# Kernel tuning notes

Hardware: AMD Instinct MI355X
Metric: run time of the kernel (lower is better)

Reference implementation:

```python
import jax, jax.numpy as jnp
import numpy as np

N = 100000   # n_nodes
E = 1000000  # n_edges
B = 2000     # batch of interactions
K = 20       # n_neighbors
D = 172      # memory/node/edge/embedding dim
T = 172      # time encoding dim
MSG = 2 * D + D + T  # 688, identity message function
HEADS = 2


def setup_inputs() -> dict:
    key = jax.random.key(0)
    ks = jax.random.split(key, 32)
    g = lambda i, shape, fan: jax.random.normal(ks[i], shape, jnp.float32) / np.float32(np.sqrt(fan))
    inp = {}
    inp['memory'] = jax.random.normal(ks[0], (N, D), jnp.float32)
    inp['messages'] = jax.random.normal(ks[1], (N, MSG), jnp.float32)
    inp['edge_features'] = jax.random.normal(ks[2], (E, D), jnp.float32)
    inp['edge_times'] = jax.random.uniform(ks[3], (B,), jnp.float32) * 10000.0
    inp['neighbor_times'] = jax.random.uniform(ks[4], (3 * B, K), jnp.float32) * 10000.0
    # TimeEncode init: w = 1 / 10^linspace(0, 9, T)
    inp['time_w'] = jnp.asarray(1.0 / 10.0 ** np.linspace(0, 9, T), jnp.float32)
    inp['time_b'] = jnp.zeros((T,), jnp.float32)
    # GRUCell params
    inp['gru_w_ih'] = g(5, (3 * D, MSG), MSG)
    inp['gru_w_hh'] = g(6, (3 * D, D), D)
    inp['gru_b_ih'] = jnp.zeros((3 * D,), jnp.float32)
    inp['gru_b_hh'] = jnp.zeros((3 * D,), jnp.float32)
    # temporal attention params: query = [feat||time], key = [feat||edge||time]
    inp['w_q'] = g(7, (D, D + T), D + T)
    inp['w_k'] = g(8, (D, D + D + T), D + D + T)
    inp['w_v'] = g(9, (D, D + D + T), D + D + T)
    inp['w_o'] = g(10, (D, D), D)
    # MergeLayer(attn_out, src_feat)
    inp['merge_w1'] = g(11, (D, 2 * D), 2 * D)
    inp['merge_b1'] = jnp.zeros((D,), jnp.float32)
    inp['merge_w2'] = g(12, (D, D), D)
    inp['merge_b2'] = jnp.zeros((D,), jnp.float32)
    # affinity MergeLayer -> scalar score
    inp['aff_w1'] = g(13, (D, 2 * D), 2 * D)
    inp['aff_b1'] = jnp.zeros((D,), jnp.float32)
    inp['aff_w2'] = g(14, (1, D), D)
    inp['aff_b2'] = jnp.zeros((1,), jnp.float32)
    inp['source_nodes'] = jax.random.randint(ks[15], (B,), 0, N, jnp.int32)
    inp['destination_nodes'] = jax.random.randint(ks[16], (B,), 0, N, jnp.int32)
    inp['negative_nodes'] = jax.random.randint(ks[17], (B,), 0, N, jnp.int32)
    inp['neighbors'] = jax.random.randint(ks[18], (3 * B, K), 0, N, jnp.int32)
    inp['neighbor_edge_idxs'] = jax.random.randint(ks[19], (3 * B, K), 0, E, jnp.int32)
    return inp


def reference(memory, messages, edge_features, edge_times, neighbor_times,
              time_w, time_b, gru_w_ih, gru_w_hh, gru_b_ih, gru_b_hh,
              w_q, w_k, w_v, w_o, merge_w1, merge_b1, merge_w2, merge_b2,
              aff_w1, aff_b1, aff_w2, aff_b2,
              source_nodes, destination_nodes, negative_nodes,
              neighbors, neighbor_edge_idxs):
    d = memory.shape[1]
    dh = d // HEADS
    k_nbr = neighbors.shape[1]

    def time_enc(t):  # TimeEncode: cos(t * w + b)
        return jnp.cos(t[..., None] * time_w + time_b)

    # --- GRU memory update from aggregated ('last') messages ---
    gi = messages @ gru_w_ih.T + gru_b_ih          # [N, 3D]
    gh = memory @ gru_w_hh.T + gru_b_hh            # [N, 3D]
    i_r, i_z, i_n = jnp.split(gi, 3, axis=-1)
    h_r, h_z, h_n = jnp.split(gh, 3, axis=-1)
    r = jax.nn.sigmoid(i_r + h_r)
    z = jax.nn.sigmoid(i_z + h_z)
    n = jnp.tanh(i_n + r * h_n)
    mem_upd = (1.0 - z) * n + z * memory           # [N, D]

    # --- temporal graph attention embedding (1 layer) ---
    nodes = jnp.concatenate([source_nodes, destination_nodes, negative_nodes])  # [3B]
    ts = jnp.concatenate([edge_times, edge_times, edge_times])                  # [3B]
    m = nodes.shape[0]
    src_feat = mem_upd[nodes]                                                   # [3B, D]
    q_in = jnp.concatenate([src_feat, time_enc(jnp.zeros_like(ts))], axis=-1)   # [3B, D+T]
    nbr_feat = mem_upd[neighbors]                                               # [3B, K, D]
    e_feat = edge_features[neighbor_edge_idxs]                                  # [3B, K, D]
    dt = ts[:, None] - neighbor_times                                           # [3B, K]
    k_in = jnp.concatenate([nbr_feat, e_feat, time_enc(dt)], axis=-1)           # [3B, K, 2D+T]

    q = (q_in @ w_q.T).reshape(m, HEADS, dh)
    kk = (k_in @ w_k.T).reshape(m, k_nbr, HEADS, dh)
    vv = (k_in @ w_v.T).reshape(m, k_nbr, HEADS, dh)
    scores = jnp.einsum('nhd,nkhd->nhk', q, kk) / np.float32(np.sqrt(dh))
    valid = (neighbors > 0)[:, None, :]            # node 0 is the pad node
    scores = jnp.where(valid, scores, jnp.float32(-1e9))
    attn = jax.nn.softmax(scores, axis=-1)
    ctx = jnp.einsum('nhk,nkhd->nhd', attn, vv).reshape(m, d) @ w_o.T
    h1 = jax.nn.relu(jnp.concatenate([ctx, src_feat], axis=-1) @ merge_w1.T + merge_b1)
    emb = h1 @ merge_w2.T + merge_b2               # [3B, D]

    # --- affinity score on (src,dst) and (src,neg) pairs ---
    b = source_nodes.shape[0]
    s_emb, d_emb, n_emb = emb[:b], emb[b:2 * b], emb[2 * b:]
    s_cat = jnp.concatenate([s_emb, s_emb], axis=0)
    d_cat = jnp.concatenate([d_emb, n_emb], axis=0)
    ah = jax.nn.relu(jnp.concatenate([s_cat, d_cat], axis=-1) @ aff_w1.T + aff_b1)
    prob = jax.nn.sigmoid((ah @ aff_w2.T + aff_b2).squeeze(-1))  # [2B]
    return prob[:b], prob[b:]
```

## Files before the change

### kernel.cpp

```cpp
#include <hip/hip_runtime.h>
#include <math.h>

#define N_NODES 100000
#define BATCH   2000
#define KNBR    20
#define DF      172
#define MSGD    688
#define M3      6000
#define DH      86
#define KIN_D   516

#define KA      864
#define JP      768
#define KREAL   860
#define KSTEPS  (KA / 32)
#define NTILES_N ((N_NODES + 127) / 128)
#define NWG_GRU (NTILES_N * 6)

#define NKV     120000
#define KP_KV   544
#define JKV     384
#define KVS     352
#define NKV_TILES ((NKV + 127) / 128)
#define NKV_ROWS (NKV_TILES * 128)
#define NWG_KV  (NKV_TILES * 3)
#define KSTEPS_KV (KP_KV / 32)

typedef __bf16 bf16x8 __attribute__((ext_vector_type(8)));
typedef __bf16 bf16x4 __attribute__((ext_vector_type(4)));
typedef float  f32x4  __attribute__((ext_vector_type(4)));

#define WPB_OFF   0
#define BP4_OFF   331776
#define WKV_OFF   332544
#define MU_OFF    436992
#define UNI_OFF   17636992
#define KV_OFF    UNI_OFF
#define QB_OFF    38756992
#define CAT_OFF   39286400
#define EMBB_OFF  40922752
#define MW1O_OFF  41812608
#define WQB_OFF   41842192
#define WM1B_OFF  41875984
#define WM2B_OFF  41909776
#define WAFFB_OFF 41928208
#define BM1P_OFF  41962000
#define BM2P_OFF  41962192
#define BAFFP_OFF 41962384
#define NODES_OFF 41962768
#define KIN_OFF   42000000

__device__ __forceinline__ float sigmoidf_(float x) { return 1.0f / (1.0f + expf(-x)); }

typedef __attribute__((address_space(1))) const void gvoid;
typedef __attribute__((address_space(3))) void svoid;
__device__ __forceinline__ void gl16(const void* g, void* l) {
    __builtin_amdgcn_global_load_lds((gvoid*)g, (svoid*)l, 16, 0, 0);
}

__global__ __launch_bounds__(256) void prep_kernel(
    const float* __restrict__ w_ih, const float* __restrict__ w_hh,
    const float* __restrict__ b_ih, const float* __restrict__ b_hh,
    __bf16* __restrict__ wpb, float* __restrict__ bp4)
{
    int idx = blockIdx.x * 256 + threadIdx.x;
    if (idx < JP * KA) {
        int j = idx / KA, k = idx - j * KA;
        int d = j >> 2, g = j & 3;
        float v = 0.f;
        if (d < DF) {
            if (g == 0) {
                if (k < MSGD) v = w_ih[d * MSGD + k];
                else if (k < KREAL) v = w_hh[d * DF + (k - MSGD)];
            } else if (g == 1) {
                if (k < MSGD) v = w_ih[(d + DF) * MSGD + k];
                else if (k < KREAL) v = w_hh[(d + DF) * DF + (k - MSGD)];
            } else if (g == 2) {
                if (k < MSGD) v = w_ih[(d + 2 * DF) * MSGD + k];
            } else {
                if (k >= MSGD && k < KREAL) v = w_hh[(d + 2 * DF) * DF + (k - MSGD)];
            }
        }
        wpb[idx] = (__bf16)v;
    }
    if (idx < JP) {
        int d = idx >> 2, g = idx & 3;
        float b = 0.f;
        if (d < DF) {
            if (g == 0) b = b_ih[d] + b_hh[d];
            else if (g == 1) b = b_ih[d + DF] + b_hh[d + DF];
            else if (g == 2) b = b_ih[d + 2 * DF];
            else            b = b_hh[d + 2 * DF];
        }
        bp4[idx] = b;
    }
}

__global__ __launch_bounds__(256) void prep_kv_kernel(
    const float* __restrict__ w_k, const float* __restrict__ w_v,
    __bf16* __restrict__ wkvb)
{
    int idx = blockIdx.x * 256 + threadIdx.x;
    if (idx < JKV * KP_KV) {
        int j = idx / KP_KV, k = idx - j * KP_KV;
        float v = 0.f;
        if (k < KIN_D) {
            if (j < DF) v = w_k[j * KIN_D + k];
            else if (j >= 192 && j < 192 + DF) v = w_v[(j - 192) * KIN_D + k];
        }
        wkvb[idx] = (__bf16)v;
    }
}

__global__ __launch_bounds__(256) void conv_kernel(
    const float* __restrict__ messages, const float* __restrict__ memory,
    __bf16* __restrict__ xb)
{
    const long total = (long)N_NODES * (KA / 8);
    for (long idx = (long)blockIdx.x * 256 + threadIdx.x; idx < total;
         idx += (long)gridDim.x * 256) {
        const int r  = (int)(idx / (KA / 8));
        const int k  = (int)(idx - (long)r * (KA / 8)) * 8;
        float f[8];
        if (k < MSGD) {
            const float4 a = *(const float4*)(messages + (size_t)r * MSGD + k);
            const float4 b = *(const float4*)(messages + (size_t)r * MSGD + k + 4);
            f[0]=a.x; f[1]=a.y; f[2]=a.z; f[3]=a.w;
            f[4]=b.x; f[5]=b.y; f[6]=b.z; f[7]=b.w;
        } else {
            const int o = k - MSGD;
            const float4 a = *(const float4*)(memory + (size_t)r * DF + o);
            float4 b = make_float4(0.f, 0.f, 0.f, 0.f);
            if (o <= 164) b = *(const float4*)(memory + (size_t)r * DF + o + 4);
            f[0]=a.x; f[1]=a.y; f[2]=a.z; f[3]=a.w;
            f[4]=b.x; f[5]=b.y; f[6]=b.z; f[7]=b.w;
        }
        bf16x8 v;
#pragma unroll
        for (int j = 0; j < 8; ++j) v[j] = (__bf16)f[j];
        *(bf16x8*)(xb + (size_t)r * KA + k) = v;
    }
}

__global__ __launch_bounds__(256) void mw1o_kernel(
    const float* __restrict__ merge_w1, const float* __restrict__ w_o,
    float* __restrict__ mw1o)
{
    int idx = blockIdx.x * 256 + threadIdx.x;
    if (idx >= DF * DF) return;
    int j = idx / DF, k = idx - j * DF;
    float s = 0.f;
    for (int c = 0; c < DF; ++c)
        s = fmaf(merge_w1[j * 344 + c], w_o[c * DF + k], s);
    mw1o[idx] = s;
}

__global__ __launch_bounds__(256) void prep_tail_kernel(
    const float* __restrict__ w_q, const float* __restrict__ mw1o,
    const float* __restrict__ merge_w1, const float* __restrict__ merge_w2,
    const float* __restrict__ aff_w1,
    const float* __restrict__ merge_b1, const float* __restrict__ merge_b2,
    const float* __restrict__ aff_b1,
    const int* __restrict__ src_nodes, const int* __restrict__ dst_nodes,
    const int* __restrict__ neg_nodes,
    __bf16* __restrict__ wqb, __bf16* __restrict__ wm1b,
    __bf16* __restrict__ wm2b, __bf16* __restrict__ waffb,
    float* __restrict__ bm1p, float* __restrict__ bm2p,
    float* __restrict__ baffp, int* __restrict__ nodes_cat)
{
    int idx = blockIdx.x * 256 + threadIdx.x;
    if (idx < 192 * 352) {
        int j = idx / 352, k = idx - j * 352;
        float vq = 0.f, vm = 0.f, va = 0.f;
        if (j < DF) {
            if (k < DF) {
                vq = w_q[j * 344 + k];
                vm = mw1o[j * DF + k];
                va = aff_w1[j * 344 + k];
            } else if (k >= 176 && k < 348) {
                vq = w_q[j * 344 + 172 + (k - 176)];
                vm = merge_w1[j * 344 + 172 + (k - 176)];
                va = aff_w1[j * 344 + 172 + (k - 176)];
            }
        }
        wqb[idx] = (__bf16)vq;
        wm1b[idx] = (__bf16)vm;
        waffb[idx] = (__bf16)va;
    }
    if (idx < 192 * 192) {
        int j = idx / 192, k = idx - j * 192;
        wm2b[idx] = (__bf16)((j < DF && k < DF) ? merge_w2[j * DF + k] : 0.f);
    }
    if (idx < 192) {
        bm1p[idx]  = (idx < DF) ? merge_b1[idx] : 0.f;
        bm2p[idx]  = (idx < DF) ? merge_b2[idx] : 0.f;
        baffp[idx] = (idx < DF) ? aff_b1[idx] : 0.f;
    }
    if (idx < 6016) {
        int i = min(idx, M3 - 1);
        int node;
        if (i < BATCH)          node = src_nodes[i];
        else if (i < 2 * BATCH) node = dst_nodes[i - BATCH];
        else                    node = neg_nodes[i - 2 * BATCH];
        nodes_cat[idx] = node;
    }
}

__global__ __launch_bounds__(512) void gru_mfma5_kernel(
    const __bf16* __restrict__ xb, const __bf16* __restrict__ wpb,
    const float* __restrict__ bp4, const float* __restrict__ memory,
    __bf16* __restrict__ mem_upd)
{
    __shared__ __align__(16) __bf16 Ws[3][128 * 32];
    __shared__ __align__(16) __bf16 Xs[3][128 * 32];

    const int t    = threadIdx.x;
    const int w    = t >> 6, lane = t & 63;
    const int lo   = lane & 15, hi = lane >> 4;
    const int wm   = w & 1;
    const int wn   = w >> 1;

    const int orig = blockIdx.x;
    const int q = NWG_GRU >> 3, rr = NWG_GRU & 7;
    const int xcd = orig & 7, oidx = orig >> 3;
    const int wgid = (xcd < rr ? xcd * (q + 1) : rr * (q + 1) + (xcd - rr) * q) + oidx;
    const int m_tile = wgid % 6;
    const int n_tile = wgid / 6;
    const int n0 = n_tile * 128;
    const int j0 = m_tile * 128;

    const int srow  = lane >> 2;
    const int sslot = ((lane & 3) ^ ((srow >> 1) & 3)) * 8;

    f32x4 acc[4][2];
#pragma unroll
    for (int mi = 0; mi < 4; ++mi)
#pragma unroll
        for (int ni = 0; ni < 2; ++ni)
            acc[mi][ni] = (f32x4){0.f, 0.f, 0.f, 0.f};

    const __bf16* wbase = wpb + (size_t)j0 * KA;
    const __bf16* xbase = xb + (size_t)n0 * KA;

#define STAGE(buf, k0)                                                          \
    {                                                                           \
        const int lr = w * 16 + srow;                                           \
        gl16(wbase + (size_t)lr * KA + (k0) + sslot, &Ws[buf][(w * 16) * 32]);  \
        gl16(xbase + (size_t)lr * KA + (k0) + sslot, &Xs[buf][(w * 16) * 32]);  \
    }

    STAGE(0, 0);
    STAGE(1, 32);

    const int fsa = (hi ^ ((lo >> 1) & 3)) * 8;
    for (int ks = 0; ks < KSTEPS; ++ks) {
        if (ks < KSTEPS - 1) {
            asm volatile("s_waitcnt vmcnt(2)" ::: "memory");
        } else {
            asm volatile("s_waitcnt vmcnt(0)" ::: "memory");
        }
        __builtin_amdgcn_s_barrier();
        if (ks + 2 < KSTEPS) STAGE((ks + 2) % 3, (ks + 2) * 32);

        const int bi = ks % 3;
        bf16x8 af[4], bx_[2];
#pragma unroll
        for (int i = 0; i < 4; ++i)
            af[i]  = *(const bf16x8*)&Ws[bi][(wm * 64 + i * 16 + lo) * 32 + fsa];
#pragma unroll
        for (int i = 0; i < 2; ++i)
            bx_[i] = *(const bf16x8*)&Xs[bi][(wn * 32 + i * 16 + lo) * 32 + fsa];
#pragma unroll
        for (int mi = 0; mi < 4; ++mi)
#pragma unroll
            for (int ni = 0; ni < 2; ++ni)
                acc[mi][ni] = __builtin_amdgcn_mfma_f32_16x16x32_bf16(
                    af[mi], bx_[ni], acc[mi][ni], 0, 0, 0);
    }
#undef STAGE

    const int dbase = m_tile * 32 + wm * 16;
#pragma unroll
    for (int mi = 0; mi < 4; ++mi) {
        const int d = dbase + mi * 4 + hi;
        if (d >= DF) continue;
        const float4 b4 = *(const float4*)&bp4[4 * d];
#pragma unroll
        for (int ni = 0; ni < 2; ++ni) {
            const int n = n0 + wn * 32 + ni * 16 + lo;
            if (n >= N_NODES) continue;
            float sr  = acc[mi][ni][0] + b4.x;
            float sz  = acc[mi][ni][1] + b4.y;
            float gin = acc[mi][ni][2] + b4.z;
            float ghn = acc[mi][ni][3] + b4.w;
            float mem = memory[(size_t)n * DF + d];
            float rg  = sigmoidf_(sr);
            float zg  = sigmoidf_(sz);
            float nt  = tanhf(fmaf(rg, ghn, gin));
            mem_upd[(size_t)n * DF + d] = (__bf16)fmaf(zg, mem - nt, nt);
        }
    }
}

__global__ __launch_bounds__(256) void kin_build_kernel(
    const __bf16* __restrict__ mem_upd, const float* __restrict__ edge_features,
    const float* __restrict__ edge_times, const float* __restrict__ neighbor_times,
    const float* __restrict__ time_w, const float* __restrict__ time_b,
    const int* __restrict__ neighbors, const int* __restrict__ nbr_eidx,
    __bf16* __restrict__ kin)
{
    const long total = (long)NKV_ROWS * 136;
    for (long idx = (long)blockIdx.x * 256 + threadIdx.x; idx < total;
         idx += (long)gridDim.x * 256) {
        const int r  = (int)(idx / 136);
        const int c  = (int)(idx - (long)r * 136) * 4;
        const int rc = min(r, NKV - 1);
        bf16x4 o;
        if (c < DF) {
            const int nbr = neighbors[rc];
            o = *(const bf16x4*)(mem_upd + (size_t)nbr * DF + c);
        } else if (c < 2 * DF) {
            const int eidx = nbr_eidx[rc];
            const float4 v = *(const float4*)(edge_features + (size_t)eidx * DF + (c - DF));
            o[0] = (__bf16)v.x; o[1] = (__bf16)v.y;
            o[2] = (__bf16)v.z; o[3] = (__bf16)v.w;
        } else if (c < KIN_D) {
            const float dt = edge_times[(rc / KNBR) % BATCH] - neighbor_times[rc];
            const float4 tw = *(const float4*)(time_w + (c - 2 * DF));
            const float4 tb = *(const float4*)(time_b + (c - 2 * DF));
            o[0] = (__bf16)cosf(fmaf(dt, tw.x, tb.x));
            o[1] = (__bf16)cosf(fmaf(dt, tw.y, tb.y));
            o[2] = (__bf16)cosf(fmaf(dt, tw.z, tb.z));
            o[3] = (__bf16)cosf(fmaf(dt, tw.w, tb.w));
        } else {
            o[0] = o[1] = o[2] = o[3] = (__bf16)0.f;
        }
        *(bf16x4*)(kin + (size_t)r * KP_KV + c) = o;
    }
}

__global__ __launch_bounds__(512) void kv_gemm4_kernel(
    const __bf16* __restrict__ kin, const __bf16* __restrict__ wkvb,
    __bf16* __restrict__ kv)
{
    __shared__ __align__(16) __bf16 Ws[3][128 * 32];
    __shared__ __align__(16) __bf16 Xs[3][128 * 32];

    const int t    = threadIdx.x;
    const int w    = t >> 6, lane = t & 63;
    const int lo   = lane & 15, hi = lane >> 4;
    const int wm   = w & 1;
    const int wn   = w >> 1;

    const int orig = blockIdx.x;
    const int q = NWG_KV >> 3, rr = NWG_KV & 7;
    const int xcd = orig & 7, oidx = orig >> 3;
    const int wgid = (xcd < rr ? xcd * (q + 1) : rr * (q + 1) + (xcd - rr) * q) + oidx;
    const int m_tile = wgid % 3;
    const int n_tile = wgid / 3;
    const int n0 = n_tile * 128;
    const int j0 = m_tile * 128;

    const int srow  = lane >> 2;
    const int sslot = ((lane & 3) ^ ((srow >> 1) & 3)) * 8;

    f32x4 acc[4][2];
#pragma unroll
    for (int mi = 0; mi < 4; ++mi)
#pragma unroll
        for (int ni = 0; ni < 2; ++ni)
            acc[mi][ni] = (f32x4){0.f, 0.f, 0.f, 0.f};

    const __bf16* wbase = wkvb + (size_t)j0 * KP_KV;
    const __bf16* xbase = kin + (size_t)n0 * KP_KV;

#define STAGE(buf, k0)                                                           \
    {                                                                            \
        const int lr = w * 16 + srow;                                            \
        gl16(wbase + (size_t)lr * KP_KV + (k0) + sslot, &Ws[buf][(w * 16) * 32]);\
        gl16(xbase + (size_t)lr * KP_KV + (k0) + sslot, &Xs[buf][(w * 16) * 32]);\
    }

    STAGE(0, 0);
    STAGE(1, 32);

    const int fsa = (hi ^ ((lo >> 1) & 3)) * 8;
    for (int ks = 0; ks < KSTEPS_KV; ++ks) {
        if (ks < KSTEPS_KV - 1) {
            asm volatile("s_waitcnt vmcnt(2)" ::: "memory");
        } else {
            asm volatile("s_waitcnt vmcnt(0)" ::: "memory");
        }
        __builtin_amdgcn_s_barrier();
        if (ks + 2 < KSTEPS_KV) STAGE((ks + 2) % 3, (ks + 2) * 32);

        const int bi = ks % 3;
        bf16x8 af[4], bx_[2];
#pragma unroll
        for (int i = 0; i < 4; ++i)
            af[i]  = *(const bf16x8*)&Ws[bi][(wm * 64 + i * 16 + lo) * 32 + fsa];
#pragma unroll
        for (int i = 0; i < 2; ++i)
            bx_[i] = *(const bf16x8*)&Xs[bi][(wn * 32 + i * 16 + lo) * 32 + fsa];
#pragma unroll
        for (int mi = 0; mi < 4; ++mi)
#pragma unroll
            for (int ni = 0; ni < 2; ++ni)
                acc[mi][ni] = __builtin_amdgcn_mfma_f32_16x16x32_bf16(
                    af[mi], bx_[ni], acc[mi][ni], 0, 0, 0);
    }
#undef STAGE

#pragma unroll
    for (int mi = 0; mi < 4; ++mi) {
        const int jb = j0 + wm * 64 + mi * 16 + hi * 4;
        int off;
        if (jb + 3 < DF)                 off = jb;
        else if (jb >= 192 && jb < 361)  off = jb - 16;
        else continue;
#pragma unroll
        for (int ni = 0; ni < 2; ++ni) {
            const int n = n0 + wn * 32 + ni * 16 + lo;
            if (n >= NKV) continue;
            bf16x4 o;
            o[0] = (__bf16)acc[mi][ni][0];
            o[1] = (__bf16)acc[mi][ni][1];
            o[2] = (__bf16)acc[mi][ni][2];
            o[3] = (__bf16)acc[mi][ni][3];
            *(bf16x4*)(kv + (size_t)n * KVS + off) = o;
        }
    }
}

__global__ __launch_bounds__(256) void q_gemm_kernel(
    const __bf16* __restrict__ wqb, const __bf16* __restrict__ mem_upd,
    const float* __restrict__ time_b, const int* __restrict__ nodes_cat,
    __bf16* __restrict__ qbuf)
{
    __shared__ __align__(16) __bf16 Ws[128][32];
    __shared__ __align__(16) __bf16 Xs[128][32];

    const int t    = threadIdx.x;
    const int w    = t >> 6, lane = t & 63;
    const int lo   = lane & 15, hi = lane >> 4;
    const int wm   = w >> 1, wn = w & 1;

    const int n_tile = blockIdx.x >> 1;
    const int j0     = (blockIdx.x & 1) * 64;
    const int n0     = n_tile * 128;

    const int xrow  = t >> 1, xhalf = t & 1;
    const int nr    = min(n0 + xrow, M3 - 1);
    const __bf16* mrow = mem_upd + (size_t)nodes_cat[nr] * DF;
    const __bf16* wrow = wqb + (size_t)(j0 + xrow) * 352;

    f32x4 acc[4][4];
#pragma unroll
    for (int mi = 0; mi < 4; ++mi)
#pragma unroll
        for (int ni = 0; ni < 4; ++ni)
            acc[mi][ni] = (f32x4){0.f, 0.f, 0.f, 0.f};

    for (int k0 = 0; k0 < 352; k0 += 32) {
        bf16x8 w0 = *(const bf16x8*)(wrow + k0 + xhalf * 16);
        bf16x8 w1 = *(const bf16x8*)(wrow + k0 + xhalf * 16 + 8);
        bf16x8 x0, x1;
#pragma unroll
        for (int c = 0; c < 4; ++c) {
            const int b = k0 + xhalf * 16 + c * 4;
            __bf16 e0, e1, e2, e3;
            if (b + 3 < DF) {
                bf16x4 h = *(const bf16x4*)(mrow + b);
                e0 = h[0]; e1 = h[1]; e2 = h[2]; e3 = h[3];
            } else if (b >= 176 && b < 348) {
                const float4 tb = *(const float4*)(time_b + (b - 176));
                e0 = (__bf16)cosf(tb.x); e1 = (__bf16)cosf(tb.y);
                e2 = (__bf16)cosf(tb.z); e3 = (__bf16)cosf(tb.w);
            } else {
                e0 = e1 = e2 = e3 = (__bf16)0.f;
            }
            if (c < 2) { x0[c*4]=e0; x0[c*4+1]=e1; x0[c*4+2]=e2; x0[c*4+3]=e3; }
            else { x1[(c-2)*4]=e0; x1[(c-2)*4+1]=e1; x1[(c-2)*4+2]=e2; x1[(c-2)*4+3]=e3; }
        }
        *(bf16x8*)&Ws[xrow][xhalf * 16]     = w0;
        *(bf16x8*)&Ws[xrow][xhalf * 16 + 8] = w1;
        *(bf16x8*)&Xs[xrow][xhalf * 16]     = x0;
        *(bf16x8*)&Xs[xrow][xhalf * 16 + 8] = x1;
        __syncthreads();

        bf16x8 af[4], bx_[4];
#pragma unroll
        for (int i = 0; i < 4; ++i) {
            af[i]  = *(const bf16x8*)&Ws[wm * 64 + i * 16 + lo][hi * 8];
            bx_[i] = *(const bf16x8*)&Xs[wn * 64 + i * 16 + lo][hi * 8];
        }
#pragma unroll
        for (int mi = 0; mi < 4; ++mi)
#pragma unroll
            for (int ni = 0; ni < 4; ++ni)
                acc[mi][ni] = __builtin_amdgcn_mfma_f32_16x16x32_bf16(
                    af[mi], bx_[ni], acc[mi][ni], 0, 0, 0);
        __syncthreads();
    }

#pragma unroll
    for (int mi = 0; mi < 4; ++mi) {
        const int jb = j0 + wm * 64 + mi * 16 + hi * 4;
        if (jb + 3 >= 176) continue;
#pragma unroll
        for (int ni = 0; ni < 4; ++ni) {
            const int n = n0 + wn * 64 + ni * 16 + lo;
            if (n >= M3) continue;
            bf16x4 o;
            o[0]=(__bf16)acc[mi][ni][0]; o[1]=(__bf16)acc[mi][ni][1];
            o[2]=(__bf16)acc[mi][ni][2]; o[3]=(__bf16)acc[mi][ni][3];
            *(bf16x4*)(qbuf + (size_t)n * 176 + jb) = o;
        }
    }
}

__global__ __launch_bounds__(256) void attn_mid_kernel(
    const __bf16* __restrict__ mem_upd, const __bf16* __restrict__ kv,
    const __bf16* __restrict__ qb, const int* __restrict__ neighbors,
    const int* __restrict__ nodes_cat, __bf16* __restrict__ cat)
{
    __shared__ __align__(16) __bf16 kvs[KNBR][KVS];
    __shared__ float qs[176];
    __shared__ float scl[2][KNBR];
    __shared__ float attnl[2][KNBR];
    __shared__ int   nbrs[KNBR];

    const int i = blockIdx.x;
    const int t = threadIdx.x;

    if (t < KNBR) nbrs[t] = neighbors[i * KNBR + t];
    if (t < 176) qs[t] = (float)qb[(size_t)i * 176 + t];
    {
        const uint4* src = (const uint4*)(kv + (size_t)i * KNBR * KVS);
        uint4* dst = (uint4*)&kvs[0][0];
        for (int idx = t; idx < KNBR * KVS / 8; idx += 256) dst[idx] = src[idx];
    }
    __syncthreads();

    if (t < 2 * KNBR) {
        int h = t / KNBR, kn = t - h * KNBR;
        float s = 0.f;
#pragma unroll 2
        for (int j = 0; j < DH; ++j)
            s = fmaf(qs[h * DH + j], (float)kvs[kn][h * DH + j], s);
        s /= sqrtf((float)DH);
        scl[h][kn] = (nbrs[kn] > 0) ? s : -1e9f;
    }
    __syncthreads();
    if (t < 2) {
        float m = -INFINITY;
        for (int kn = 0; kn < KNBR; ++kn) m = fmaxf(m, scl[t][kn]);
        float se = 0.f;
        for (int kn = 0; kn < KNBR; ++kn) se += expf(scl[t][kn] - m);
        float inv = 1.f / se;
        for (int kn = 0; kn < KNBR; ++kn) attnl[t][kn] = expf(scl[t][kn] - m) * inv;
    }
    __syncthreads();
    if (t < DF) {
        int h = t / DH;
        float cx = 0.f;
#pragma unroll
        for (int kn = 0; kn < KNBR; ++kn)
            cx = fmaf(attnl[h][kn], (float)kvs[kn][176 + t], cx);
        cat[(size_t)i * 352 + t] = (__bf16)cx;
        cat[(size_t)i * 352 + 176 + t] = mem_upd[(size_t)nodes_cat[i] * DF + t];
    }
    if (t < 4) {
        cat[(size_t)i * 352 + 172 + t] = (__bf16)0.f;
        cat[(size_t)i * 352 + 348 + t] = (__bf16)0.f;
    }
}

__global__ __launch_bounds__(256) void merge_emb_kernel(
    const __bf16* __restrict__ cat, const __bf16* __restrict__ wm1b,
    const __bf16* __restrict__ wm2b, const float* __restrict__ bm1p,
    const float* __restrict__ bm2p, __bf16* __restrict__ embb)
{
    __shared__ __align__(16) __bf16 Ws[192 * 32];
    __shared__ __align__(16) __bf16 Xs[128 * 32];
    __shared__ __align__(16) __bf16 h1[128 * 200];

    const int t    = threadIdx.x;
    const int w    = t >> 6, lane = t & 63;
    const int lo   = lane & 15, hi = lane >> 4;
    const int wm   = w >> 1, wn = w & 1;
    const int n0   = blockIdx.x * 128;

    const int srow  = lane >> 2;
    const int sslot = ((lane & 3) ^ ((lane >> 3) & 3)) * 8;
    const int fsa   = (hi ^ ((lo >> 1) & 3)) * 8;

    f32x4 acc[6][4];
#pragma unroll
    for (int mi = 0; mi < 6; ++mi)
#pragma unroll
        for (int ni = 0; ni < 4; ++ni)
            acc[mi][ni] = (f32x4){0.f, 0.f, 0.f, 0.f};

    for (int k0 = 0; k0 < 352; k0 += 32) {
#pragma unroll
        for (int qq = 0; qq < 3; ++qq) {
            const int jr = w * 48 + qq * 16 + srow;
            gl16(wm1b + (size_t)jr * 352 + k0 + sslot, &Ws[(w * 48 + qq * 16) * 32]);
        }
#pragma unroll
        for (int qq = 0; qq < 2; ++qq) {
            const int r = w * 32 + qq * 16 + srow;
            const int nr = min(n0 + r, M3 - 1);
            gl16(cat + (size_t)nr * 352 + k0 + sslot, &Xs[(w * 32 + qq * 16) * 32]);
        }
        asm volatile("s_waitcnt vmcnt(0)" ::: "memory");
        __syncthreads();

        bf16x8 af[6], bx_[4];
#pragma unroll
        for (int i = 0; i < 6; ++i)
            af[i] = *(const bf16x8*)&Ws[(wm * 96 + i * 16 + lo) * 32 + fsa];
#pragma unroll
        for (int i = 0; i < 4; ++i)
            bx_[i] = *(const bf16x8*)&Xs[(wn * 64 + i * 16 + lo) * 32 + fsa];
#pragma unroll
        for (int mi = 0; mi < 6; ++mi)
#pragma unroll
            for (int ni = 0; ni < 4; ++ni)
                acc[mi][ni] = __builtin_amdgcn_mfma_f32_16x16x32_bf16(
                    af[mi], bx_[ni], acc[mi][ni], 0, 0, 0);
        __syncthreads();
    }

#pragma unroll
    for (int mi = 0; mi < 6; ++mi) {
        const int jb = wm * 96 + mi * 16 + hi * 4;
        const float4 b4 = *(const float4*)(bm1p + jb);
#pragma unroll
        for (int ni = 0; ni < 4; ++ni) {
            const int nl = wn * 64 + ni * 16 + lo;
            bf16x4 o;
            o[0] = (__bf16)fmaxf(acc[mi][ni][0] + b4.x, 0.f);
            o[1] = (__bf16)fmaxf(acc[mi][ni][1] + b4.y, 0.f);
            o[2] = (__bf16)fmaxf(acc[mi][ni][2] + b4.z, 0.f);
            o[3] = (__bf16)fmaxf(acc[mi][ni][3] + b4.w, 0.f);
            *(bf16x4*)&h1[nl * 200 + jb] = o;
        }
    }
    __syncthreads();

    f32x4 acc2[6][4];
#pragma unroll
    for (int mi = 0; mi < 6; ++mi)
#pragma unroll
        for (int ni = 0; ni < 4; ++ni)
            acc2[mi][ni] = (f32x4){0.f, 0.f, 0.f, 0.f};

    for (int k0 = 0; k0 < 192; k0 += 32) {
#pragma unroll
        for (int qq = 0; qq < 3; ++qq) {
            const int jr = w * 48 + qq * 16 + srow;
            gl16(wm2b + (size_t)jr * 192 + k0 + sslot, &Ws[(w * 48 + qq * 16) * 32]);
        }
        asm volatile("s_waitcnt vmcnt(0)" ::: "memory");
        __syncthreads();

        bf16x8 af[6], bx_[4];
#pragma unroll
        for (int i = 0; i < 6; ++i)
            af[i] = *(const bf16x8*)&Ws[(wm * 96 + i * 16 + lo) * 32 + fsa];
#pragma unroll
        for (int i = 0; i < 4; ++i)
            bx_[i] = *(const bf16x8*)&h1[(wn * 64 + i * 16 + lo) * 200 + k0 + hi * 8];
#pragma unroll
        for (int mi = 0; mi < 6; ++mi)
#pragma unroll
            for (int ni = 0; ni < 4; ++ni)
                acc2[mi][ni] = __builtin_amdgcn_mfma_f32_16x16x32_bf16(
                    af[mi], bx_[ni], acc2[mi][ni], 0, 0, 0);
        __syncthreads();
    }

#pragma unroll
    for (int mi = 0; mi < 6; ++mi) {
        const int jb = wm * 96 + mi * 16 + hi * 4;
        if (jb + 3 >= 176) continue;
        const float4 b4 = *(const float4*)(bm2p + jb);
#pragma unroll
        for (int ni = 0; ni < 4; ++ni) {
            const int n = n0 + wn * 64 + ni * 16 + lo;
            if (n >= M3) continue;
            bf16x4 o;
            o[0] = (__bf16)(acc2[mi][ni][0] + b4.x);
            o[1] = (__bf16)(acc2[mi][ni][1] + b4.y);
            o[2] = (__bf16)(acc2[mi][ni][2] + b4.z);
            o[3] = (__bf16)(acc2[mi][ni][3] + b4.w);
            *(bf16x4*)(embb + (size_t)n * 176 + jb) = o;
        }
    }
}

__global__ __launch_bounds__(256) void aff_fused_kernel(
    const __bf16* __restrict__ embb, const __bf16* __restrict__ waffb,
    const float* __restrict__ baffp, const float* __restrict__ aff_w2,
    const float* __restrict__ aff_b2, float* __restrict__ out)
{
    __shared__ __align__(16) __bf16 Ws[192 * 32];
    __shared__ __align__(16) __bf16 Xs[128 * 32];
    __shared__ float sred[2][2][4][16];

    const int t    = threadIdx.x;
    const int w    = t >> 6, lane = t & 63;
    const int lo   = lane & 15, hi = lane >> 4;
    const int wm   = w >> 1, wn = w & 1;
    const int n0   = blockIdx.x * 128;

    const int srow  = lane >> 2;
    const int sslot = ((lane & 3) ^ ((lane >> 3) & 3)) * 8;
    const int fsa   = (hi ^ ((lo >> 1) & 3)) * 8;

    f32x4 acc[6][4];
#pragma unroll
    for (int mi = 0; mi < 6; ++mi)
#pragma unroll
        for (int ni = 0; ni < 4; ++ni)
            acc[mi][ni] = (f32x4){0.f, 0.f, 0.f, 0.f};

    for (int k0 = 0; k0 < 352; k0 += 32) {
#pragma unroll
        for (int qq = 0; qq < 3; ++qq) {
            const int jr = w * 48 + qq * 16 + srow;
            gl16(waffb + (size_t)jr * 352 + k0 + sslot, &Ws[(w * 48 + qq * 16) * 32]);
        }
#pragma unroll
        for (int qq = 0; qq < 2; ++qq) {
            const int r = w * 32 + qq * 16 + srow;
            const int nr = min(n0 + r, 2 * BATCH - 1);
            const int s  = (nr < BATCH) ? nr : nr - BATCH;
            const int col = k0 + sslot;
            const __bf16* src = (col < 176)
                ? embb + (size_t)s * 176 + col
                : embb + (size_t)(nr + BATCH) * 176 + (col - 176);
            gl16(src, &Xs[(w * 32 + qq * 16) * 32]);
        }
        asm volatile("s_waitcnt vmcnt(0)" ::: "memory");
        __syncthreads();

        bf16x8 af[6], bx_[4];
#pragma unroll
        for (int i = 0; i < 6; ++i)
            af[i] = *(const bf16x8*)&Ws[(wm * 96 + i * 16 + lo) * 32 + fsa];
#pragma unroll
        for (int i = 0; i < 4; ++i)
            bx_[i] = *(const bf16x8*)&Xs[(wn * 64 + i * 16 + lo) * 32 + fsa];
#pragma unroll
        for (int mi = 0; mi < 6; ++mi)
#pragma unroll
            for (int ni = 0; ni < 4; ++ni)
                acc[mi][ni] = __builtin_amdgcn_mfma_f32_16x16x32_bf16(
                    af[mi], bx_[ni], acc[mi][ni], 0, 0, 0);
        __syncthreads();
    }

    float ps[4] = {0.f, 0.f, 0.f, 0.f};
#pragma unroll
    for (int mi = 0; mi < 6; ++mi) {
        const int jb = wm * 96 + mi * 16 + hi * 4;
#pragma unroll
        for (int r = 0; r < 4; ++r) {
            const int j = jb + r;
            const float w2v = (j < DF) ? aff_w2[j] : 0.f;
            const float bb  = baffp[j];
#pragma unroll
            for (int ni = 0; ni < 4; ++ni)
                ps[ni] += fmaxf(acc[mi][ni][r] + bb, 0.f) * w2v;
        }
    }
#pragma unroll
    for (int ni = 0; ni < 4; ++ni) {
        ps[ni] += __shfl_xor(ps[ni], 16, 64);
        ps[ni] += __shfl_xor(ps[ni], 32, 64);
    }
    if (hi == 0) {
#pragma unroll
        for (int ni = 0; ni < 4; ++ni) sred[wm][wn][ni][lo] = ps[ni];
    }
    __syncthreads();
    if (t < 128) {
        const int n = n0 + t;
        if (n < 2 * BATCH) {
            const int wn2 = t >> 6, ni = (t >> 4) & 3, lo2 = t & 15;
            float s = sred[0][wn2][ni][lo2] + sred[1][wn2][ni][lo2] + aff_b2[0];
            out[n] = 1.f / (1.f + expf(-s));
        }
    }
}

extern "C" void kernel_launch(void* const* d_in, const int* in_sizes, int n_in,
                              void* d_out, int out_size, void* d_ws, size_t ws_size,
                              hipStream_t stream)
{
    (void)in_sizes; (void)n_in; (void)out_size; (void)ws_size;
    const float* memory         = (const float*)d_in[0];
    const float* messages       = (const float*)d_in[1];
    const float* edge_features  = (const float*)d_in[2];
    const float* edge_times     = (const float*)d_in[3];
    const float* neighbor_times = (const float*)d_in[4];
    const float* time_w         = (const float*)d_in[5];
    const float* time_b         = (const float*)d_in[6];
    const float* gru_w_ih       = (const float*)d_in[7];
    const float* gru_w_hh       = (const float*)d_in[8];
    const float* gru_b_ih       = (const float*)d_in[9];
    const float* gru_b_hh       = (const float*)d_in[10];
    const float* w_q            = (const float*)d_in[11];
    const float* w_k            = (const float*)d_in[12];
    const float* w_v            = (const float*)d_in[13];
    const float* w_o            = (const float*)d_in[14];
    const float* merge_w1       = (const float*)d_in[15];
    const float* merge_b1       = (const float*)d_in[16];
    const float* merge_w2       = (const float*)d_in[17];
    const float* merge_b2       = (const float*)d_in[18];
    const float* aff_w1         = (const float*)d_in[19];
    const float* aff_b1         = (const float*)d_in[20];
    const float* aff_w2         = (const float*)d_in[21];
    const float* aff_b2         = (const float*)d_in[22];
    const int* src_nodes        = (const int*)d_in[23];
    const int* dst_nodes        = (const int*)d_in[24];
    const int* neg_nodes        = (const int*)d_in[25];
    const int* neighbors        = (const int*)d_in[26];
    const int* nbr_eidx         = (const int*)d_in[27];

    float* ws       = (float*)d_ws;
    __bf16* wpb     = (__bf16*)(ws + WPB_OFF);
    float* bp4      = ws + BP4_OFF;
    __bf16* wkvb    = (__bf16*)(ws + WKV_OFF);
    __bf16* mem_upd = (__bf16*)(ws + MU_OFF);
    __bf16* xbuf    = (__bf16*)(ws + UNI_OFF);
    __bf16* kv      = (__bf16*)(ws + KV_OFF);
    __bf16* qbuf    = (__bf16*)(ws + QB_OFF);
    __bf16* cat     = (__bf16*)(ws + CAT_OFF);
    __bf16* embb    = (__bf16*)(ws + EMBB_OFF);
    float* mw1o     = ws + MW1O_OFF;
    __bf16* wqb     = (__bf16*)(ws + WQB_OFF);
    __bf16* wm1b    = (__bf16*)(ws + WM1B_OFF);
    __bf16* wm2b    = (__bf16*)(ws + WM2B_OFF);
    __bf16* waffb   = (__bf16*)(ws + WAFFB_OFF);
    float* bm1p     = ws + BM1P_OFF;
    float* bm2p     = ws + BM2P_OFF;
    float* baffp    = ws + BAFFP_OFF;
    int*   nodes_cat= (int*)(ws + NODES_OFF);
    __bf16* kin     = (__bf16*)(ws + KIN_OFF);
    float* out      = (float*)d_out;

    prep_kernel<<<(JP * KA + 255) / 256, 256, 0, stream>>>(
        gru_w_ih, gru_w_hh, gru_b_ih, gru_b_hh, wpb, bp4);
    prep_kv_kernel<<<(JKV * KP_KV + 255) / 256, 256, 0, stream>>>(w_k, w_v, wkvb);
    conv_kernel<<<2048, 256, 0, stream>>>(messages, memory, xbuf);
    gru_mfma5_kernel<<<NWG_GRU, 512, 0, stream>>>(xbuf, wpb, bp4, memory, mem_upd);
    mw1o_kernel<<<(DF * DF + 255) / 256, 256, 0, stream>>>(merge_w1, w_o, mw1o);
    prep_tail_kernel<<<(192 * 352 + 255) / 256, 256, 0, stream>>>(
        w_q, mw1o, merge_w1, merge_w2, aff_w1, merge_b1, merge_b2, aff_b1,
        src_nodes, dst_nodes, neg_nodes,
        wqb, wm1b, wm2b, waffb, bm1p, bm2p, baffp, nodes_cat);
    kin_build_kernel<<<2048, 256, 0, stream>>>(
        mem_upd, edge_features, edge_times, neighbor_times, time_w, time_b,
        neighbors, nbr_eidx, kin);
    kv_gemm4_kernel<<<NWG_KV, 512, 0, stream>>>(kin, wkvb, kv);
    q_gemm_kernel<<<47 * 2, 256, 0, stream>>>(wqb, mem_upd, time_b, nodes_cat, qbuf);
    attn_mid_kernel<<<M3, 256, 0, stream>>>(
        mem_upd, kv, qbuf, neighbors, nodes_cat, cat);
    merge_emb_kernel<<<47, 256, 0, stream>>>(cat, wm1b, wm2b, bm1p, bm2p, embb);
    aff_fused_kernel<<<32, 256, 0, stream>>>(embb, waffb, baffp, aff_w2, aff_b2, out);
}
```

Baseline: 644.6 us.

## Retile tail GEMMs, batch two rows per attention block, reuse bf16 memory in GRU

The GRU epilogue now reads the previous memory from the bf16 staging buffer instead of the fp32 memory array, which cuts a separate global read but lowers the precision of the carried state. The Q GEMM covers all 192 output rows per block with async LDS loads and swizzling rather than splitting the output across two blocks. The attention kernel handles two nodes per block to halve the launch count. The merge GEMM uses 64-row tiles to double the grid size, and the LDS swizzle slot formula is changed in several kernels.

New measurement: 635.7 us. About the same (-1.4%).

```diff
diff --git a/kernel.cpp b/kernel.cpp
--- a/kernel.cpp
+++ b/kernel.cpp
@@ -208,8 +208,7 @@
 
 __global__ __launch_bounds__(512) void gru_mfma5_kernel(
     const __bf16* __restrict__ xb, const __bf16* __restrict__ wpb,
-    const float* __restrict__ bp4, const float* __restrict__ memory,
-    __bf16* __restrict__ mem_upd)
+    const float* __restrict__ bp4, __bf16* __restrict__ mem_upd)
 {
     __shared__ __align__(16) __bf16 Ws[3][128 * 32];
     __shared__ __align__(16) __bf16 Xs[3][128 * 32];
@@ -293,7 +292,7 @@
             float sz  = acc[mi][ni][1] + b4.y;
             float gin = acc[mi][ni][2] + b4.z;
             float ghn = acc[mi][ni][3] + b4.w;
-            float mem = memory[(size_t)n * DF + d];
+            float mem = (float)xb[(size_t)n * KA + MSGD + d];
             float rg  = sigmoidf_(sr);
             float zg  = sigmoidf_(sz);
             float nt  = tanhf(fmaf(rg, ghn, gin));
@@ -437,33 +436,36 @@
     const float* __restrict__ time_b, const int* __restrict__ nodes_cat,
     __bf16* __restrict__ qbuf)
 {
-    __shared__ __align__(16) __bf16 Ws[128][32];
+    __shared__ __align__(16) __bf16 Ws[192 * 32];
     __shared__ __align__(16) __bf16 Xs[128][32];
 
     const int t    = threadIdx.x;
     const int w    = t >> 6, lane = t & 63;
     const int lo   = lane & 15, hi = lane >> 4;
     const int wm   = w >> 1, wn = w & 1;
-
-    const int n_tile = blockIdx.x >> 1;
-    const int j0     = (blockIdx.x & 1) * 64;
-    const int n0     = n_tile * 128;
+    const int n0   = blockIdx.x * 128;
 
     const int xrow  = t >> 1, xhalf = t & 1;
     const int nr    = min(n0 + xrow, M3 - 1);
     const __bf16* mrow = mem_upd + (size_t)nodes_cat[nr] * DF;
-    const __bf16* wrow = wqb + (size_t)(j0 + xrow) * 352;
-
-    f32x4 acc[4][4];
-#pragma unroll
-    for (int mi = 0; mi < 4; ++mi)
+
+    const int srow  = lane >> 2;
+    const int sslot = ((lane & 3) ^ ((srow >> 1) & 3)) * 8;
+    const int fsa   = (hi ^ ((lo >> 1) & 3)) * 8;
+
+    f32x4 acc[6][4];
+#pragma unroll
+    for (int mi = 0; mi < 6; ++mi)
 #pragma unroll
         for (int ni = 0; ni < 4; ++ni)
             acc[mi][ni] = (f32x4){0.f, 0.f, 0.f, 0.f};
 
     for (int k0 = 0; k0 < 352; k0 += 32) {
-        bf16x8 w0 = *(const bf16x8*)(wrow + k0 + xhalf * 16);
-        bf16x8 w1 = *(const bf16x8*)(wrow + k0 + xhalf * 16 + 8);
+#pragma unroll
+        for (int qq = 0; qq < 3; ++qq) {
+            const int jr = w * 48 + qq * 16 + srow;
+            gl16(wqb + (size_t)jr * 352 + k0 + sslot, &Ws[(w * 48 + qq * 16) * 32]);
+        }
         bf16x8 x0, x1;
 #pragma unroll
         for (int c = 0; c < 4; ++c) {
@@ -482,20 +484,19 @@
             if (c < 2) { x0[c*4]=e0; x0[c*4+1]=e1; x0[c*4+2]=e2; x0[c*4+3]=e3; }
             else { x1[(c-2)*4]=e0; x1[(c-2)*4+1]=e1; x1[(c-2)*4+2]=e2; x1[(c-2)*4+3]=e3; }
         }
-        *(bf16x8*)&Ws[xrow][xhalf * 16]     = w0;
-        *(bf16x8*)&Ws[xrow][xhalf * 16 + 8] = w1;
         *(bf16x8*)&Xs[xrow][xhalf * 16]     = x0;
         *(bf16x8*)&Xs[xrow][xhalf * 16 + 8] = x1;
         __syncthreads();
 
-        bf16x8 af[4], bx_[4];
-#pragma unroll
-        for (int i = 0; i < 4; ++i) {
-            af[i]  = *(const bf16x8*)&Ws[wm * 64 + i * 16 + lo][hi * 8];
+        bf16x8 af[6], bx_[4];
+#pragma unroll
+        for (int i = 0; i < 6; ++i)
+            af[i] = *(const bf16x8*)&Ws[(wm * 96 + i * 16 + lo) * 32 + fsa];
+#pragma unroll
+        for (int i = 0; i < 4; ++i)
             bx_[i] = *(const bf16x8*)&Xs[wn * 64 + i * 16 + lo][hi * 8];
-        }
-#pragma unroll
-        for (int mi = 0; mi < 4; ++mi)
+#pragma unroll
+        for (int mi = 0; mi < 6; ++mi)
 #pragma unroll
             for (int ni = 0; ni < 4; ++ni)
                 acc[mi][ni] = __builtin_amdgcn_mfma_f32_16x16x32_bf16(
@@ -504,8 +505,8 @@
     }
 
 #pragma unroll
-    for (int mi = 0; mi < 4; ++mi) {
-        const int jb = j0 + wm * 64 + mi * 16 + hi * 4;
+    for (int mi = 0; mi < 6; ++mi) {
+        const int jb = wm * 96 + mi * 16 + hi * 4;
         if (jb + 3 >= 176) continue;
 #pragma unroll
         for (int ni = 0; ni < 4; ++ni) {
@@ -524,55 +525,68 @@
     const __bf16* __restrict__ qb, const int* __restrict__ neighbors,
     const int* __restrict__ nodes_cat, __bf16* __restrict__ cat)
 {
-    __shared__ __align__(16) __bf16 kvs[KNBR][KVS];
-    __shared__ float qs[176];
-    __shared__ float scl[2][KNBR];
-    __shared__ float attnl[2][KNBR];
-    __shared__ int   nbrs[KNBR];
-
-    const int i = blockIdx.x;
+    __shared__ __align__(16) __bf16 kvs[2][KNBR][KVS];
+    __shared__ float qs[2][176];
+    __shared__ float scl[2][2][KNBR];
+    __shared__ float attnl[2][2][KNBR];
+    __shared__ int   nbrs[2][KNBR];
+
+    const int i0 = blockIdx.x * 2;
     const int t = threadIdx.x;
 
-    if (t < KNBR) nbrs[t] = neighbors[i * KNBR + t];
-    if (t < 176) qs[t] = (float)qb[(size_t)i * 176 + t];
+    if (t < 2 * KNBR) {
+        int q = t / KNBR, kn = t - q * KNBR;
+        nbrs[q][kn] = neighbors[(i0 + q) * KNBR + kn];
+    }
+    for (int idx = t; idx < 352; idx += 256) {
+        int q = idx / 176, c = idx - q * 176;
+        qs[q][c] = (float)qb[(size_t)(i0 + q) * 176 + c];
+    }
     {
-        const uint4* src = (const uint4*)(kv + (size_t)i * KNBR * KVS);
-        uint4* dst = (uint4*)&kvs[0][0];
-        for (int idx = t; idx < KNBR * KVS / 8; idx += 256) dst[idx] = src[idx];
+        const uint4* src = (const uint4*)(kv + (size_t)i0 * KNBR * KVS);
+        uint4* dst = (uint4*)&kvs[0][0][0];
+        for (int idx = t; idx < 2 * KNBR * KVS / 8; idx += 256) dst[idx] = src[idx];
     }
     __syncthreads();
 
-    if (t < 2 * KNBR) {
-        int h = t / KNBR, kn = t - h * KNBR;
+    if (t < 4 * KNBR) {
+        int q = t / (2 * KNBR);
+        int r = t - q * 2 * KNBR;
+        int h = r / KNBR, kn = r - h * KNBR;
         float s = 0.f;
 #pragma unroll 2
         for (int j = 0; j < DH; ++j)
-            s = fmaf(qs[h * DH + j], (float)kvs[kn][h * DH + j], s);
+            s = fmaf(qs[q][h * DH + j], (float)kvs[q][kn][h * DH + j], s);
         s /= sqrtf((float)DH);
-        scl[h][kn] = (nbrs[kn] > 0) ? s : -1e9f;
+        scl[q][h][kn] = (nbrs[q][kn] > 0) ? s : -1e9f;
     }
     __syncthreads();
-    if (t < 2) {
+    if (t < 4) {
+        int q = t >> 1, h = t & 1;
         float m = -INFINITY;
-        for (int kn = 0; kn < KNBR; ++kn) m = fmaxf(m, scl[t][kn]);
+        for (int kn = 0; kn < KNBR; ++kn) m = fmaxf(m, scl[q][h][kn]);
         float se = 0.f;
-        for (int kn = 0; kn < KNBR; ++kn) se += expf(scl[t][kn] - m);
+        for (int kn = 0; kn < KNBR; ++kn) se += expf(scl[q][h][kn] - m);
         float inv = 1.f / se;
-        for (int kn = 0; kn < KNBR; ++kn) attnl[t][kn] = expf(scl[t][kn] - m) * inv;
+        for (int kn = 0; kn < KNBR; ++kn)
+            attnl[q][h][kn] = expf(scl[q][h][kn] - m) * inv;
     }
     __syncthreads();
-    if (t < DF) {
-        int h = t / DH;
+    for (int idx = t; idx < 2 * DF; idx += 256) {
+        int q = idx / DF, d = idx - q * DF;
+        int h = d / DH;
         float cx = 0.f;
 #pragma unroll
         for (int kn = 0; kn < KNBR; ++kn)
-            cx = fmaf(attnl[h][kn], (float)kvs[kn][176 + t], cx);
-        cat[(size_t)i * 352 + t] = (__bf16)cx;
-        cat[(size_t)i * 352 + 176 + t] = mem_upd[(size_t)nodes_cat[i] * DF + t];
-    }
-    if (t < 4) {
-        cat[(size_t)i * 352 + 172 + t] = (__bf16)0.f;
-        cat[(size_t)i * 352 + 348 + t] = (__bf16)0.f;
+            cx = fmaf(attnl[q][h][kn], (float)kvs[q][kn][176 + d], cx);
+        cat[(size_t)(i0 + q) * 352 + d] = (__bf16)cx;
+        cat[(size_t)(i0 + q) * 352 + 176 + d] =
+            mem_upd[(size_t)nodes_cat[i0 + q] * DF + d];
+    }
+    if (t < 8) {
+        int q = t >> 2, r = t & 3;
+        cat[(size_t)(i0 + q) * 352 + 172 + r] = (__bf16)0.f;
+        cat[(size_t)(i0 + q) * 352 + 348 + r] = (__bf16)0.f;
     }
 }
 
@@ -582,24 +596,24 @@
     const float* __restrict__ bm2p, __bf16* __restrict__ embb)
 {
     __shared__ __align__(16) __bf16 Ws[192 * 32];
-    __shared__ __align__(16) __bf16 Xs[128 * 32];
-    __shared__ __align__(16) __bf16 h1[128 * 200];
+    __shared__ __align__(16) __bf16 Xs[64 * 32];
+    __shared__ __align__(16) __bf16 h1[64 * 200];
 
     const int t    = threadIdx.x;
     const int w    = t >> 6, lane = t & 63;
     const int lo   = lane & 15, hi = lane >> 4;
     const int wm   = w >> 1, wn = w & 1;
-    const int n0   = blockIdx.x * 128;
+    const int n0   = blockIdx.x * 64;
 
     const int srow  = lane >> 2;
-    const int sslot = ((lane & 3) ^ ((lane >> 3) & 3)) * 8;
+    const int sslot = ((lane & 3) ^ ((srow >> 1) & 3)) * 8;
     const int fsa   = (hi ^ ((lo >> 1) & 3)) * 8;
 
-    f32x4 acc[6][4];
+    f32x4 acc[6][2];
 #pragma unroll
     for (int mi = 0; mi < 6; ++mi)
 #pragma unroll
-        for (int ni = 0; ni < 4; ++ni)
+        for (int ni = 0; ni < 2; ++ni)
             acc[mi][ni] = (f32x4){0.f, 0.f, 0.f, 0.f};
 
     for (int k0 = 0; k0 < 352; k0 += 32) {
@@ -608,26 +622,25 @@
             const int jr = w * 48 + qq * 16 + srow;
             gl16(wm1b + (size_t)jr * 352 + k0 + sslot, &Ws[(w * 48 + qq * 16) * 32]);
         }
-#pragma unroll
-        for (int qq = 0; qq < 2; ++qq) {
-            const int r = w * 32 + qq * 16 + srow;
+        {
+            const int r = w * 16 + srow;
             const int nr = min(n0 + r, M3 - 1);
-            gl16(cat + (size_t)nr * 352 + k0 + sslot, &Xs[(w * 32 + qq * 16) * 32]);
+            gl16(cat + (size_t)nr * 352 + k0 + sslot, &Xs[(w * 16) * 32]);
         }
         asm volatile("s_waitcnt vmcnt(0)" ::: "memory");
         __syncthreads();
 
-        bf16x8 af[6], bx_[4];
+        bf16x8 af[6], bx_[2];
 #pragma unroll
         for (int i = 0; i < 6; ++i)
             af[i] = *(const bf16x8*)&Ws[(wm * 96 + i * 16 + lo) * 32 + fsa];
 #pragma unroll
-        for (int i = 0; i < 4; ++i)
-            bx_[i] = *(const bf16x8*)&Xs[(wn * 64 + i * 16 + lo) * 32 + fsa];
+        for (int i = 0; i < 2; ++i)
+            bx_[i] = *(const bf16x8*)&Xs[(wn * 32 + i * 16 + lo) * 32 + fsa];
 #pragma unroll
         for (int mi = 0; mi < 6; ++mi)
 #pragma unroll
-            for (int ni = 0; ni < 4; ++ni)
+            for (int ni = 0; ni < 2; ++ni)
                 acc[mi][ni] = __builtin_amdgcn_mfma_f32_16x16x32_bf16(
                     af[mi], bx_[ni], acc[mi][ni], 0, 0, 0);
         __syncthreads();
@@ -638,8 +651,8 @@
         const int jb = wm * 96 + mi * 16 + hi * 4;
         const float4 b4 = *(const float4*)(bm1p + jb);
 #pragma unroll
-        for (int ni = 0; ni < 4; ++ni) {
-            const int nl = wn * 64 + ni * 16 + lo;
+        for (int ni = 0; ni < 2; ++ni) {
+            const int nl = wn * 32 + ni * 16 + lo;
             bf16x4 o;
             o[0] = (__bf16)fmaxf(acc[mi][ni][0] + b4.x, 0.f);
             o[1] = (__bf16)fmaxf(acc[mi][ni][1] + b4.y, 0.f);
@@ -650,11 +663,11 @@
     }
     __syncthreads();
 
-    f32x4 acc2[6][4];
+    f32x4 acc2[6][2];
 #pragma unroll
     for (int mi = 0; mi < 6; ++mi)
 #pragma unroll
-        for (int ni = 0; ni < 4; ++ni)
+        for (int ni = 0; ni < 2; ++ni)
             acc2[mi][ni] = (f32x4){0.f, 0.f, 0.f, 0.f};
 
     for (int k0 = 0; k0 < 192; k0 += 32) {
@@ -666,17 +679,17 @@
         asm volatile("s_waitcnt vmcnt(0)" ::: "memory");
         __syncthreads();
 
-        bf16x8 af[6], bx_[4];
+        bf16x8 af[6], bx_[2];
 #pragma unroll
         for (int i = 0; i < 6; ++i)
             af[i] = *(const bf16x8*)&Ws[(wm * 96 + i * 16 + lo) * 32 + fsa];
 #pragma unroll
-        for (int i = 0; i < 4; ++i)
-            bx_[i] = *(const bf16x8*)&h1[(wn * 64 + i * 16 + lo) * 200 + k0 + hi * 8];
+        for (int i = 0; i < 2; ++i)
+            bx_[i] = *(const bf16x8*)&h1[(wn * 32 + i * 16 + lo) * 200 + k0 + hi * 8];
 #pragma unroll
         for (int mi = 0; mi < 6; ++mi)
 #pragma unroll
-            for (int ni = 0; ni < 4; ++ni)
+            for (int ni = 0; ni < 2; ++ni)
                 acc2[mi][ni] = __builtin_amdgcn_mfma_f32_16x16x32_bf16(
                     af[mi], bx_[ni], acc2[mi][ni], 0, 0, 0);
         __syncthreads();
@@ -688,8 +701,8 @@
         if (jb + 3 >= 176) continue;
         const float4 b4 = *(const float4*)(bm2p + jb);
 #pragma unroll
-        for (int ni = 0; ni < 4; ++ni) {
-            const int n = n0 + wn * 64 + ni * 16 + lo;
+        for (int ni = 0; ni < 2; ++ni) {
+            const int n = n0 + wn * 32 + ni * 16 + lo;
             if (n >= M3) continue;
             bf16x4 o;
             o[0] = (__bf16)(acc2[mi][ni][0] + b4.x);
@@ -717,7 +730,7 @@
     const int n0   = blockIdx.x * 128;
 
     const int srow  = lane >> 2;
-    const int sslot = ((lane & 3) ^ ((lane >> 3) & 3)) * 8;
+    const int sslot = ((lane & 3) ^ ((srow >> 1) & 3)) * 8;
     const int fsa   = (hi ^ ((lo >> 1) & 3)) * 8;
 
     f32x4 acc[6][4];
@@ -857,7 +870,7 @@
         gru_w_ih, gru_w_hh, gru_b_ih, gru_b_hh, wpb, bp4);
     prep_kv_kernel<<<(JKV * KP_KV + 255) / 256, 256, 0, stream>>>(w_k, w_v, wkvb);
     conv_kernel<<<2048, 256, 0, stream>>>(messages, memory, xbuf);
-    gru_mfma5_kernel<<<NWG_GRU, 512, 0, stream>>>(xbuf, wpb, bp4, memory, mem_upd);
+    gru_mfma5_kernel<<<NWG_GRU, 512, 0, stream>>>(xbuf, wpb, bp4, mem_upd);
     mw1o_kernel<<<(DF * DF + 255) / 256, 256, 0, stream>>>(merge_w1, w_o, mw1o);
     prep_tail_kernel<<<(192 * 352 + 255) / 256, 256, 0, stream>>>(
         w_q, mw1o, merge_w1, merge_w2, aff_w1, merge_b1, merge_b2, aff_b1,
@@ -867,9 +880,9 @@
         mem_upd, edge_features, edge_times, neighbor_times, time_w, time_b,
         neighbors, nbr_eidx, kin);
     kv_gemm4_kernel<<<NWG_KV, 512, 0, stream>>>(kin, wkvb, kv);
-    q_gemm_kernel<<<47 * 2, 256, 0, stream>>>(wqb, mem_upd, time_b, nodes_cat, qbuf);
-    attn_mid_kernel<<<M3, 256, 0, stream>>>(
+    q_gemm_kernel<<<47, 256, 0, stream>>>(wqb, mem_upd, time_b, nodes_cat, qbuf);
+    attn_mid_kernel<<<M3 / 2, 256, 0, stream>>>(
         mem_upd, kv, qbuf, neighbors, nodes_cat, cat);
-    merge_emb_kernel<<<47, 256, 0, stream>>>(cat, wm1b, wm2b, bm1p, bm2p, embb);
+    merge_emb_kernel<<<94, 256, 0, stream>>>(cat, wm1b, wm2b, bm1p, bm2p, embb);
     aff_fused_kernel<<<32, 256, 0, stream>>>(embb, waffb, baffp, aff_w2, aff_b2, out);
 }
```
